# Kernel optimization log

Measured on AMD Instinct MI355X. Metric: run time of the kernel, lower is better.

## Reference

```python
import jax, jax.numpy as jnp
import numpy as np

N, T = 64, 256
TOTAL_NODES, C_IN = 25, 128          # c = 3200
NUM_SEEDS, C_OUT = 5, 3              # seeds flat dim = 15
NEW_NODES = 20
LIN_IN = TOTAL_NODES * C_IN + NUM_SEEDS * C_OUT  # 3215


def setup_inputs() -> dict:
    key = jax.random.key(0)
    k1, k2, k3 = jax.random.split(key, 3)
    x = jax.random.normal(k1, (N, T, TOTAL_NODES * C_IN), dtype=jnp.float32)
    seeds = jax.random.normal(k2, (N, T, NUM_SEEDS, C_OUT), dtype=jnp.float32)
    # Stacked weights of the `new_nodes` cloned Linear(LIN_IN, C_OUT) layers.
    W = jax.random.normal(k3, (NEW_NODES, C_OUT, LIN_IN), dtype=jnp.float32) * 0.02
    b = jnp.zeros((NEW_NODES, C_OUT), dtype=jnp.float32)
    return {"x": x, "seeds": seeds, "W": W, "b": b}


def reference(x, seeds, W, b):
    n, t, _ = x.shape
    mix = jnp.concatenate([x, seeds.reshape(n, t, -1)], axis=2)  # [n,t,LIN_IN]
    # Fuse all cloned small Linears into one batched GEMM, then layout as
    # torch.stack([...], dim=3): output [n, t, c_out, new_nodes].
    out = jnp.einsum('ntc,koc->ntok', mix, W) + b.T  # b.T: [c_out, new_nodes]
    return out
```

## Files before the change

### kernel.cpp

```cpp
#include <hip/hip_runtime.h>


#define NROWS    16384
#define CIN      3200
#define SEED_K   15
#define LIN_IN   3215
#define NCOL     60
#define KB_MAIN  100
#define WB_ELEMS ((KB_MAIN + 1) * 4 * 64 * 8)
#define NCHUNKS  100
#define DEPTH    6
#define SLOT_SZ  4096
#define B_BASE   32768
#define SMEM_SZ  65536

typedef __attribute__((ext_vector_type(8))) __bf16 bf16x8;
typedef __attribute__((ext_vector_type(4))) float f32x4;
typedef __attribute__((ext_vector_type(8))) unsigned short ushort8;

__device__ unsigned short Wb_g[WB_ELEMS];
__device__ __align__(16) float bias_g[64];

__device__ inline unsigned short f2bf_rne(float f) {
    unsigned int u = __builtin_bit_cast(unsigned int, f);
    u += 0x7fffu + ((u >> 16) & 1u);
    return (unsigned short)(u >> 16);
}

__device__ inline bf16x8 to_bf16x8(f32x4 a0, f32x4 a1) {
    ushort8 u;
    u[0] = f2bf_rne(a0[0]); u[1] = f2bf_rne(a0[1]);
    u[2] = f2bf_rne(a0[2]); u[3] = f2bf_rne(a0[3]);
    u[4] = f2bf_rne(a1[0]); u[5] = f2bf_rne(a1[1]);
    u[6] = f2bf_rne(a1[2]); u[7] = f2bf_rne(a1[3]);
    return __builtin_bit_cast(bf16x8, u);
}

typedef __attribute__((address_space(3))) void lds_void;
typedef __attribute__((address_space(1))) const void gm_void;
__device__ __forceinline__ void gll16(const void* g, void* l) {
    __builtin_amdgcn_global_load_lds((gm_void*)g, (lds_void*)l, 16, 0, 0);
}

#define VB(N) asm volatile("s_waitcnt vmcnt(" #N ")\n\ts_barrier" ::: "memory")

__global__ void prep_B(const float* __restrict__ W, const float* __restrict__ b) {
    int idx = blockIdx.x * blockDim.x + threadIdx.x;
    if (idx >= WB_ELEMS) return;
    if (idx < 64) bias_g[idx] = (idx < NCOL) ? b[(idx % 20) * 3 + (idx / 20)] : 0.f;
    int jj   = idx & 7;
    int lane = (idx >> 3) & 63;
    int nt   = (idx >> 9) & 3;
    int kb   = idx >> 11;
    int k = kb * 32 + (lane >> 4) * 8 + jj;
    int n = nt * 16 + (lane & 15);
    float v = 0.0f;
    if (k < LIN_IN && n < NCOL) {
        int o = n / 20, kn = n % 20;
        v = W[(kn * 3 + o) * LIN_IN + k];
    }
    Wb_g[idx] = f2bf_rne(v);
}

__global__ __launch_bounds__(256) void gen_nodes(
    const float* __restrict__ x, const float* __restrict__ seeds,
    float* __restrict__ out) {
    const int lane = threadIdx.x & 63;
    const int wave = threadIdx.x >> 6;
    const int quad = lane >> 4;
    const int l15  = lane & 15;
    const int rb0  = blockIdx.x * 32;
    const int wt   = wave & 1;
    const int nh   = wave >> 1;

    __shared__ __align__(16) char smem[SMEM_SZ];

    const float* aSrc = x + (size_t)(rb0 + (wave >> 1) * 16 + l15) * CIN
                          + quad * 8 + (wave & 1) * 4;
    const unsigned short* bSrc = Wb_g + wave * 512 + lane * 8;

    f32x4 acc[2];
    acc[0] = (f32x4){0.f, 0.f, 0.f, 0.f};
    acc[1] = (f32x4){0.f, 0.f, 0.f, 0.f};

    auto stage = [&](int cbk) {
        int slot = cbk & 7;
        gll16(aSrc + (size_t)cbk * 32, smem + slot * SLOT_SZ + wave * 1024);
        gll16(bSrc + (size_t)cbk * 2048,
              smem + B_BASE + slot * SLOT_SZ + wave * 1024);
    };

#pragma unroll
    for (int c0 = 0; c0 < DEPTH; ++c0) stage(c0);

    for (int c = 0; c < NCHUNKS; ++c) {
        if (c + DEPTH < NCHUNKS) {
            stage(c + DEPTH);
            VB(12);
        } else {
            int ah = NCHUNKS - 1 - c;
            if      (ah >= 5) VB(10);
            else if (ah == 4) VB(8);
            else if (ah == 3) VB(6);
            else if (ah == 2) VB(4);
            else if (ah == 1) VB(2);
            else              VB(0);
        }

        const int slot = c & 7;
        const char* ab = smem + slot * SLOT_SZ + wt * 2048 + lane * 16;
        f32x4 a0 = *(const f32x4*)(ab);
        f32x4 a1 = *(const f32x4*)(ab + 1024);
        const char* bb = smem + B_BASE + slot * SLOT_SZ + nh * 2048 + lane * 16;
        bf16x8 b0 = *(const bf16x8*)(bb);
        bf16x8 b1 = *(const bf16x8*)(bb + 1024);
        bf16x8 af = to_bf16x8(a0, a1);
        acc[0] = __builtin_amdgcn_mfma_f32_16x16x32_bf16(af, b0, acc[0], 0, 0, 0);
        acc[1] = __builtin_amdgcn_mfma_f32_16x16x32_bf16(af, b1, acc[1], 0, 0, 0);
    }

    {
        const float* srow = seeds + (size_t)(rb0 + wt * 16 + l15) * SEED_K;
        f32x4 s0 = {0.f, 0.f, 0.f, 0.f}, s1 = {0.f, 0.f, 0.f, 0.f};
#pragma unroll
        for (int j = 0; j < 4; ++j) {
            int cc = quad * 8 + j;
            if (cc < SEED_K) s0[j] = srow[cc];
            if (cc + 4 < SEED_K) s1[j] = srow[cc + 4];
        }
        bf16x8 af = to_bf16x8(s0, s1);
        const unsigned short* bb = Wb_g + (size_t)KB_MAIN * 2048 + lane * 8;
        bf16x8 b0 = *(const bf16x8*)(bb + nh * 1024);
        bf16x8 b1 = *(const bf16x8*)(bb + nh * 1024 + 512);
        acc[0] = __builtin_amdgcn_mfma_f32_16x16x32_bf16(af, b0, acc[0], 0, 0, 0);
        acc[1] = __builtin_amdgcn_mfma_f32_16x16x32_bf16(af, b1, acc[1], 0, 0, 0);
    }

#pragma unroll
    for (int t = 0; t < 2; ++t) {
        int j = (nh * 2 + t) * 16 + l15;
        if (j < NCOL) {
            float bias = bias_g[j];
#pragma unroll
            for (int r = 0; r < 4; ++r) {
                int m = wt * 16 + quad * 4 + r;
                out[(size_t)(rb0 + m) * NCOL + j] = acc[t][r] + bias;
            }
        }
    }
}

extern "C" void kernel_launch(void* const* d_in, const int* in_sizes, int n_in,
                              void* d_out, int out_size, void* d_ws, size_t ws_size,
                              hipStream_t stream) {
    const float* x     = (const float*)d_in[0];
    const float* seeds = (const float*)d_in[1];
    const float* W     = (const float*)d_in[2];
    const float* b     = (const float*)d_in[3];
    float* out = (float*)d_out;
    (void)d_ws; (void)ws_size;

    prep_B<<<(WB_ELEMS + 255) / 256, 256, 0, stream>>>(W, b);
    gen_nodes<<<NROWS / 32, 256, 0, stream>>>(x, seeds, out);
}
```

Measured before the change: 299.3 us.

## Stage A tiles as contiguous 256B row segments with XOR-swizzled LDS layout

Reorganizes the global-to-LDS staging so each row load fetches a contiguous 256-byte segment of x (64 floats, two K-chunks) instead of scattered 16-byte pieces. LDS writes are XOR-swizzled and reads are unswizzled to avoid bank conflicts. The pipeline is restructured into 50 pair-steps with 4 slots and a prefetch depth of 2. The aim is better coalescing of global loads on the bandwidth-bound x stream, at the cost of a shallower prefetch depth.

```diff
diff --git a/kernel.cpp b/kernel.cpp
--- a/kernel.cpp
+++ b/kernel.cpp
@@ -8,9 +8,8 @@
 #define NCOL     60
 #define KB_MAIN  100
 #define WB_ELEMS ((KB_MAIN + 1) * 4 * 64 * 8)
-#define NCHUNKS  100
-#define DEPTH    6
-#define SLOT_SZ  4096
+#define NPAIRS   50
+#define SLOT_SZ  8192
 #define B_BASE   32768
 #define SMEM_SZ  65536
 
@@ -75,52 +74,62 @@
 
     __shared__ __align__(16) char smem[SMEM_SZ];
 
-    const float* aSrc = x + (size_t)(rb0 + (wave >> 1) * 16 + l15) * CIN
-                          + quad * 8 + (wave & 1) * 4;
-    const unsigned short* bSrc = Wb_g + wave * 512 + lane * 8;
+    const int r4 = lane >> 4;
+    const int sw = (wave * 4 + r4) & 7;
+    const int pp = (lane & 15) ^ sw;
+    const float* aS0 = x + (size_t)(rb0 + wave * 4 + r4) * CIN + pp * 4;
+    const float* aS1 = aS0 + (size_t)16 * CIN;
+    const unsigned short* bS = Wb_g + wave * 512 + lane * 8;
 
     f32x4 acc[2];
     acc[0] = (f32x4){0.f, 0.f, 0.f, 0.f};
     acc[1] = (f32x4){0.f, 0.f, 0.f, 0.f};
 
-    auto stage = [&](int cbk) {
-        int slot = cbk & 7;
-        gll16(aSrc + (size_t)cbk * 32, smem + slot * SLOT_SZ + wave * 1024);
-        gll16(bSrc + (size_t)cbk * 2048,
-              smem + B_BASE + slot * SLOT_SZ + wave * 1024);
+    auto stage = [&](int cp) {
+        const int slot = cp & 3;
+        char* ad = smem + slot * SLOT_SZ + wave * 1024 + lane * 16;
+        gll16(aS0 + (size_t)cp * 64, ad);
+        gll16(aS1 + (size_t)cp * 64, ad + 4096);
+        char* bd = smem + B_BASE + slot * SLOT_SZ + wave * 1024 + lane * 16;
+        gll16(bS + (size_t)(2 * cp) * 2048, bd);
+        gll16(bS + (size_t)(2 * cp + 1) * 2048, bd + 4096);
     };
 
-#pragma unroll
-    for (int c0 = 0; c0 < DEPTH; ++c0) stage(c0);
+    stage(0);
+    stage(1);
 
-    for (int c = 0; c < NCHUNKS; ++c) {
-        if (c + DEPTH < NCHUNKS) {
-            stage(c + DEPTH);
-            VB(12);
+    const int mrow = wt * 16 + l15;
+    const int srd  = l15 & 7;
+    const char* arow_lds = smem + mrow * 256;
+    const char* bcol_lds = smem + B_BASE + nh * 2048 + lane * 16;
+
+    for (int cp = 0; cp < NPAIRS; ++cp) {
+        if (cp + 2 < NPAIRS) {
+            stage(cp + 2);
+            VB(8);
+        } else if (cp + 2 == NPAIRS) {
+            VB(4);
         } else {
-            int ah = NCHUNKS - 1 - c;
-            if      (ah >= 5) VB(10);
-            else if (ah == 4) VB(8);
-            else if (ah == 3) VB(6);
-            else if (ah == 2) VB(4);
-            else if (ah == 1) VB(2);
-            else              VB(0);
+            VB(0);
         }
 
-        const int slot = c & 7;
-        const char* ab = smem + slot * SLOT_SZ + wt * 2048 + lane * 16;
-        f32x4 a0 = *(const f32x4*)(ab);
-        f32x4 a1 = *(const f32x4*)(ab + 1024);
-        const char* bb = smem + B_BASE + slot * SLOT_SZ + nh * 2048 + lane * 16;
-        bf16x8 b0 = *(const bf16x8*)(bb);
-        bf16x8 b1 = *(const bf16x8*)(bb + 1024);
-        bf16x8 af = to_bf16x8(a0, a1);
-        acc[0] = __builtin_amdgcn_mfma_f32_16x16x32_bf16(af, b0, acc[0], 0, 0, 0);
-        acc[1] = __builtin_amdgcn_mfma_f32_16x16x32_bf16(af, b1, acc[1], 0, 0, 0);
+        const int sb = (cp & 3) * SLOT_SZ;
+#pragma unroll
+        for (int i = 0; i < 2; ++i) {
+            const int p0 = quad * 2 + i * 8;
+            f32x4 a0 = *(const f32x4*)(arow_lds + sb + ((p0)     ^ srd) * 16);
+            f32x4 a1 = *(const f32x4*)(arow_lds + sb + ((p0 + 1) ^ srd) * 16);
+            const char* bb = bcol_lds + sb + i * 4096;
+            bf16x8 b0 = *(const bf16x8*)(bb);
+            bf16x8 b1 = *(const bf16x8*)(bb + 1024);
+            bf16x8 af = to_bf16x8(a0, a1);
+            acc[0] = __builtin_amdgcn_mfma_f32_16x16x32_bf16(af, b0, acc[0], 0, 0, 0);
+            acc[1] = __builtin_amdgcn_mfma_f32_16x16x32_bf16(af, b1, acc[1], 0, 0, 0);
+        }
     }
 
     {
-        const float* srow = seeds + (size_t)(rb0 + wt * 16 + l15) * SEED_K;
+        const float* srow = seeds + (size_t)(rb0 + mrow) * SEED_K;
         f32x4 s0 = {0.f, 0.f, 0.f, 0.f}, s1 = {0.f, 0.f, 0.f, 0.f};
 #pragma unroll
         for (int j = 0; j < 4; ++j) {
```

Result: faster. 289.7 us (-3.2%).
